# Optimization experiments

Hardware: AMD Instinct MI355X
Metric: run time of the kernel (lower is better)

Reference implementation:

```python
import jax, jax.numpy as jnp
import numpy as np

N = 50000
E = 800000
D_IN_X = 128
D_IN = 256   # concat(x, state)
D_OUT = 128
H_EDGE = 16
EW_MAX = 5.0
EPS = 1e-06


def setup_inputs() -> dict:
    key = jax.random.key(0)
    ks = jax.random.split(key, 10)
    x = jax.random.normal(ks[0], (N, D_IN_X), dtype=jnp.float32)
    state = jax.random.normal(ks[1], (N, D_IN_X), dtype=jnp.float32)
    edge_index = jax.random.randint(ks[2], (2, E), 0, N, dtype=jnp.int64)
    edge_weight = jax.random.uniform(ks[3], (E,), dtype=jnp.float32)
    s_in = 1.0 / np.sqrt(D_IN)
    s_h = 1.0 / np.sqrt(D_OUT)
    s_o = 1.0 / np.sqrt(H_EDGE)
    W_in = jax.random.uniform(ks[4], (D_IN, D_OUT), jnp.float32, -s_in, s_in)
    b_in = jax.random.uniform(ks[5], (D_OUT,), jnp.float32, -s_in, s_in)
    W1 = jax.random.uniform(ks[6], (D_OUT, H_EDGE), jnp.float32, -s_h, s_h)
    b1 = jax.random.uniform(ks[7], (H_EDGE,), jnp.float32, -s_h, s_h)
    W2 = jax.random.uniform(ks[8], (H_EDGE, 1), jnp.float32, -s_o, s_o)
    b2 = jax.random.uniform(ks[9], (1,), jnp.float32, -s_o, s_o)
    return {"x": x, "state": state, "edge_index": edge_index, "edge_weight": edge_weight,
            "W_in": W_in, "b_in": b_in, "W1": W1, "b1": b1, "W2": W2, "b2": b2}


def reference(x, state, edge_index, edge_weight, W_in, b_in, W1, b1, W2, b2):
    n = x.shape[0]
    # node projection on concat(x, state): [N, D_OUT]
    x_proj = jnp.concatenate([x, state], axis=-1) @ W_in + b_in
    src = edge_index[0]
    dst = edge_index[1]
    msg = x_proj[src]                                   # [E, D_OUT] gather
    # dynamic edge gating: small MLP -> sigmoid -> softplus window
    h = jax.nn.leaky_relu(msg @ W1 + b1, 0.1)           # [E, 16]
    w_dyn = jax.nn.sigmoid(h @ W2 + b2)                 # [E, 1]
    w = edge_weight[:, None] * jax.nn.softplus(4.0 * (w_dyn - 0.5))
    w = jnp.clip(w, 0.0, EW_MAX)                        # (second clamp is a no-op)
    msg = msg * w
    # scatter-add aggregation + degree normalization
    out = jax.ops.segment_sum(msg, dst, num_segments=n)
    deg = jax.ops.segment_sum(jnp.abs(w), dst, num_segments=n)
    out = out / (deg + EPS)
    out = out + x_proj                                  # residual (dims match)
    out = jax.nn.gelu(out, approximate=False)           # torch nn.GELU default = exact
    return out
```

## Files before the change

kernel.cpp:

```cpp
#include <hip/hip_runtime.h>
#include <hip/hip_fp16.h>
#include <math.h>

#define NN 50000
#define NE 800000
#define DD 128
#define KIN 256
#define SCAN_BLOCKS ((NN + 255) / 256)
#define GATE_BLOCKS ((NN + 63) / 64)
#define WCONV_BLOCKS 136
#define EDGE_BLOCKS (NE / 256)

typedef __attribute__((ext_vector_type(8))) short short8;
typedef __attribute__((ext_vector_type(4))) float f32x4;

__device__ __forceinline__ float gelu_exact(float v) {
    return 0.5f * v * (1.0f + erff(v * 0.7071067811865476f));
}
__device__ __forceinline__ unsigned short f2bf(float f) {
    unsigned int u = __float_as_uint(f);
    unsigned int r = (u + 0x7fffu + ((u >> 16) & 1u)) >> 16;
    return (unsigned short)r;
}
__device__ __forceinline__ float bfhi(unsigned int v) { return __uint_as_float(v & 0xffff0000u); }
__device__ __forceinline__ float bflo(unsigned int v) { return __uint_as_float(v << 16); }

__device__ __forceinline__ unsigned pack_sw(int src, float w) {
    unsigned short h = __half_as_ushort(__float2half_rn(w));
    return ((unsigned)src << 16) | (unsigned)h;
}
__device__ __forceinline__ float unpack_w(unsigned sw) {
    return __half2float(__ushort_as_half((unsigned short)(sw & 0xffffu)));
}

__global__ __launch_bounds__(256) void prep_kernel(
    const float* __restrict__ W, const float* __restrict__ W1,
    unsigned short* __restrict__ Wt, unsigned short* __restrict__ W1t,
    const int* __restrict__ ei, int* __restrict__ hist8)
{
    const int bid = blockIdx.x, t = threadIdx.x;
    if (bid < WCONV_BLOCKS) {
        int idx = bid * 256 + t;
        if (idx < 128 * 256) {
            int c = idx >> 8, k = idx & 255;
            Wt[idx] = f2bf(W[k * 128 + c]);
        } else if (idx < 128 * 256 + 16 * 128) {
            int i = idx - 128 * 256;
            int j = i >> 7, k = i & 127;
            W1t[i] = f2bf(W1[k * 16 + j]);
        }
    } else {
        int bid2 = bid - WCONV_BLOCKS;
        int e = bid2 * 256 + t;
        int part = bid2 & 7;
        atomicAdd(&hist8[part * NN + ei[NE + e]], 1);
    }
}

__global__ __launch_bounds__(256) void proj_mfma_kernel(
    const float* __restrict__ x, const float* __restrict__ st,
    const unsigned short* __restrict__ Wt, const float* __restrict__ b,
    unsigned short* __restrict__ xpb)
{
    __shared__ unsigned short Ald[64 * 256];
    __shared__ unsigned short Bld[128 * 128];
    const int t = threadIdx.x;
    const int lane = t & 63;
    const int w = t >> 6;
    const int row0 = blockIdx.x * 64;

    #pragma unroll
    for (int i = 0; i < 8; ++i) {
        int r = i * 8 + (t >> 5);
        int kf = (t & 31) * 8;
        int grow = row0 + r;
        float v[8];
        if (grow < NN) {
            const float* src = (kf < 128) ? &x[(size_t)grow * 128 + kf]
                                          : &st[(size_t)grow * 128 + (kf - 128)];
            float4 p0 = *(const float4*)src;
            float4 p1 = *(const float4*)(src + 4);
            v[0]=p0.x; v[1]=p0.y; v[2]=p0.z; v[3]=p0.w;
            v[4]=p1.x; v[5]=p1.y; v[6]=p1.z; v[7]=p1.w;
        } else {
            #pragma unroll
            for (int j = 0; j < 8; ++j) v[j] = 0.f;
        }
        short8 h;
        #pragma unroll
        for (int j = 0; j < 8; ++j) h[j] = (short)f2bf(v[j]);
        int byte = (r * 512 + kf * 2) ^ ((r & 7) << 4);
        *(short8*)((char*)Ald + byte) = h;
    }

    auto stageB = [&](int kh) {
        #pragma unroll
        for (int i = 0; i < 8; ++i) {
            int c  = i * 16 + (t >> 4);
            int kq = (t & 15) * 8;
            short8 vv = *(const short8*)&Wt[c * 256 + kh * 128 + kq];
            int byte = (c * 256 + kq * 2) ^ ((c & 7) << 4);
            *(short8*)((char*)Bld + byte) = vv;
        }
    };
    stageB(0);
    __syncthreads();

    f32x4 acc[8];
    #pragma unroll
    for (int ct = 0; ct < 8; ++ct) acc[ct] = (f32x4){0.f, 0.f, 0.f, 0.f};

    const int arow = w * 16 + (lane & 15);
    const int kgrp = (lane >> 4) * 8;
    const int cl   = lane & 15;

    #pragma unroll
    for (int kh = 0; kh < 2; ++kh) {
        if (kh == 1) {
            __syncthreads();
            stageB(1);
            __syncthreads();
        }
        #pragma unroll
        for (int k0 = 0; k0 < 128; k0 += 32) {
            int ka = kh * 128 + k0 + kgrp;
            int abyte = (arow * 512 + ka * 2) ^ ((arow & 7) << 4);
            short8 av = *(short8*)((char*)Ald + abyte);
            #pragma unroll
            for (int ct = 0; ct < 8; ++ct) {
                int c = ct * 16 + cl;
                int bbyte = (c * 256 + (k0 + kgrp) * 2) ^ ((c & 7) << 4);
                short8 bv = *(short8*)((char*)Bld + bbyte);
                acc[ct] = __builtin_amdgcn_mfma_f32_16x16x32_bf16(av, bv, acc[ct], 0, 0, 0);
            }
        }
    }

    const int rbase = row0 + w * 16 + ((lane >> 4) << 2);
    #pragma unroll
    for (int ct = 0; ct < 8; ++ct) {
        int col = ct * 16 + cl;
        float bias = b[col];
        #pragma unroll
        for (int r = 0; r < 4; ++r) {
            int row = rbase + r;
            if (row < NN)
                xpb[(size_t)row * 128 + col] = f2bf(acc[ct][r] + bias);
        }
    }
}

__global__ __launch_bounds__(256) void gate_scan_kernel(
    const unsigned short* __restrict__ xpb, const unsigned short* __restrict__ W1t,
    const float* __restrict__ b1, const float* __restrict__ W2,
    const float* __restrict__ b2, float* __restrict__ f,
    const int* __restrict__ hist8, int* __restrict__ row_start, int* __restrict__ bsum)
{
    __shared__ int lds[256];
    const int t = threadIdx.x;
    if (blockIdx.x < GATE_BLOCKS) {
        const int lane = t & 63, w = t >> 6;
        const int base = blockIdx.x * 64 + w * 16;
        if (base >= NN) return;
        const int m  = lane & 15;
        const int kg = (lane >> 4) * 8;

        int arow = base + m;
        if (arow >= NN) arow = NN - 1;
        const unsigned short* ap = &xpb[(size_t)arow * 128 + kg];
        const unsigned short* bp = &W1t[m * 128 + kg];

        f32x4 acc = (f32x4){0.f, 0.f, 0.f, 0.f};
        #pragma unroll
        for (int k0 = 0; k0 < 4; ++k0) {
            short8 av = *(const short8*)(ap + k0 * 32);
            short8 bv = *(const short8*)(bp + k0 * 32);
            acc = __builtin_amdgcn_mfma_f32_16x16x32_bf16(av, bv, acc, 0, 0, 0);
        }

        const float bias = b1[m];
        const float w2   = W2[m];
        float zp[4];
        #pragma unroll
        for (int r = 0; r < 4; ++r) {
            float h = acc[r] + bias;
            h = (h > 0.f) ? h : 0.1f * h;
            zp[r] = h * w2;
        }
        #pragma unroll
        for (int off = 1; off <= 8; off <<= 1) {
            #pragma unroll
            for (int r = 0; r < 4; ++r)
                zp[r] += __shfl_xor(zp[r], off);
        }
        if (m == 0) {
            const float bb2 = b2[0];
            #pragma unroll
            for (int r = 0; r < 4; ++r) {
                int node = base + ((lane >> 4) << 2) + r;
                if (node < NN) {
                    float z   = zp[r] + bb2;
                    float wd  = 1.f / (1.f + expf(-z));
                    float arg = 4.f * (wd - 0.5f);
                    f[node] = log1pf(expf(arg));
                }
            }
        }
    } else {
        const int sbid = blockIdx.x - GATE_BLOCKS;
        int i = sbid * 256 + t;
        int v = 0;
        if (i < NN) {
            #pragma unroll
            for (int k = 0; k < 8; ++k) v += hist8[k * NN + i];
        }
        lds[t] = v;
        __syncthreads();
        #pragma unroll
        for (int off = 1; off < 256; off <<= 1) {
            int u = (t >= off) ? lds[t - off] : 0;
            __syncthreads();
            lds[t] += u;
            __syncthreads();
        }
        if (i < NN) row_start[i] = lds[t] - v;
        if (t == 255) bsum[sbid] = lds[255];
    }
}

__global__ __launch_bounds__(256) void scan3_kernel(
    int* __restrict__ row_start, const int* __restrict__ bsum,
    int* __restrict__ hist8 , int* __restrict__ row_end)
{
    __shared__ int lds[256];
    const int t = threadIdx.x;
    int v = (t < SCAN_BLOCKS) ? bsum[t] : 0;
    lds[t] = v;
    __syncthreads();
    #pragma unroll
    for (int off = 1; off < 256; off <<= 1) {
        int u = (t >= off) ? lds[t - off] : 0;
        __syncthreads();
        lds[t] += u;
        __syncthreads();
    }
    int boff = (blockIdx.x == 0) ? 0 : lds[blockIdx.x - 1];
    int i = blockIdx.x * 256 + t;
    if (i < NN) {
        int run = row_start[i] + boff;
        row_start[i] = run;
        #pragma unroll
        for (int k = 0; k < 8; ++k) {
            int h = hist8[k * NN + i];
            hist8[k * NN + i] = run;
            run += h;
        }
        row_end[i] = run;
    }
}

__global__ __launch_bounds__(256) void scatter_kernel(
    const int* __restrict__ ei, const float* __restrict__ ew,
    const float* __restrict__ f, int* __restrict__ cursor8,
    unsigned* __restrict__ sw_s)
{
    int e = blockIdx.x * 256 + threadIdx.x;
    int part = blockIdx.x & 7;
    int src = ei[e];
    int dst = ei[NE + e];
    float w = fminf(ew[e] * f[src], 5.0f);
    int pos = atomicAdd(&cursor8[part * NN + dst], 1);
    sw_s[pos] = pack_sw(src, w);
}

__global__ __launch_bounds__(256) void aggregate_kernel(
    const int* __restrict__ row_start, const int* __restrict__ row_end,
    const unsigned* __restrict__ sw_s, const unsigned short* __restrict__ xpb,
    float* __restrict__ out)
{
    const int wid = threadIdx.x >> 6, lane = threadIdx.x & 63;
    const int g = lane >> 4;
    const int s16 = lane & 15;
    const int n = blockIdx.x * 4 + wid;
    if (n >= NN) return;
    const int beg = row_start[n], end = row_end[n];

    float a0=0.f,a1=0.f,a2=0.f,a3=0.f,a4=0.f,a5=0.f,a6=0.f,a7=0.f,deg=0.f;

    #pragma unroll 4
    for (int i = beg; i < end; i += 4) {
        int idx = i + g;
        int idc = (idx < NE) ? idx : (NE - 1);
        unsigned sw = sw_s[idc];
        float w = (idx < end) ? unpack_w(sw) : 0.f;
        uint4 v = *(const uint4*)&xpb[(size_t)(sw >> 16) * 128 + s16 * 8];
        a0 = fmaf(bflo(v.x), w, a0);
        a1 = fmaf(bfhi(v.x), w, a1);
        a2 = fmaf(bflo(v.y), w, a2);
        a3 = fmaf(bfhi(v.y), w, a3);
        a4 = fmaf(bflo(v.z), w, a4);
        a5 = fmaf(bfhi(v.z), w, a5);
        a6 = fmaf(bflo(v.w), w, a6);
        a7 = fmaf(bfhi(v.w), w, a7);
        deg += w;
    }
    #pragma unroll
    for (int off = 16; off <= 32; off <<= 1) {
        a0 += __shfl_xor(a0, off); a1 += __shfl_xor(a1, off);
        a2 += __shfl_xor(a2, off); a3 += __shfl_xor(a3, off);
        a4 += __shfl_xor(a4, off); a5 += __shfl_xor(a5, off);
        a6 += __shfl_xor(a6, off); a7 += __shfl_xor(a7, off);
        deg += __shfl_xor(deg, off);
    }

    float inv = 1.f / (deg + 1e-6f);
    float e0 = (g == 0) ? a0 : (g == 1) ? a2 : (g == 2) ? a4 : a6;
    float e1 = (g == 0) ? a1 : (g == 1) ? a3 : (g == 2) ? a5 : a7;
    unsigned int rv = *(const unsigned int*)&xpb[(size_t)n * 128 + s16 * 8 + g * 2];
    float2 o;
    o.x = gelu_exact(fmaf(e0, inv, bflo(rv)));
    o.y = gelu_exact(fmaf(e1, inv, bfhi(rv)));
    *(float2*)&out[(size_t)n * 128 + s16 * 8 + g * 2] = o;
}

extern "C" void kernel_launch(void* const* d_in, const int* in_sizes, int n_in,
                              void* d_out, int out_size, void* d_ws, size_t ws_size,
                              hipStream_t stream)
{
    const float* x    = (const float*)d_in[0];
    const float* st   = (const float*)d_in[1];
    const int*   ei   = (const int*)d_in[2];
    const float* ew   = (const float*)d_in[3];
    const float* W_in = (const float*)d_in[4];
    const float* b_in = (const float*)d_in[5];
    const float* W1   = (const float*)d_in[6];
    const float* b1   = (const float*)d_in[7];
    const float* W2   = (const float*)d_in[8];
    const float* b2   = (const float*)d_in[9];
    float* out = (float*)d_out;

    unsigned short* xpb = (unsigned short*)d_ws;
    float* f         = (float*)(xpb + (size_t)NN * 128);
    int*   row_end   = (int*)(f + NN);
    int*   row_start = row_end + NN;
    int*   bsum      = row_start + NN;
    int*   hist8     = bsum + 256;
    unsigned* sw_s   = (unsigned*)(hist8 + 8 * NN);
    unsigned short* Wt  = (unsigned short*)(sw_s + NE);
    unsigned short* W1t = Wt + 128 * 256;

    hipMemsetAsync(hist8, 0, 8 * NN * sizeof(int), stream);

    hipLaunchKernelGGL(prep_kernel, dim3(WCONV_BLOCKS + EDGE_BLOCKS), dim3(256), 0, stream,
                       W_in, W1, Wt, W1t, ei, hist8);
    hipLaunchKernelGGL(proj_mfma_kernel, dim3((NN + 63) / 64), dim3(256), 0, stream,
                       x, st, Wt, b_in, xpb);
    hipLaunchKernelGGL(gate_scan_kernel, dim3(GATE_BLOCKS + SCAN_BLOCKS), dim3(256), 0, stream,
                       xpb, W1t, b1, W2, b2, f, hist8, row_start, bsum);
    hipLaunchKernelGGL(scan3_kernel, dim3(SCAN_BLOCKS), dim3(256), 0, stream,
                       row_start, bsum, hist8, row_end);
    hipLaunchKernelGGL(scatter_kernel, dim3(EDGE_BLOCKS), dim3(256), 0, stream,
                       ei, ew, f, hist8, sw_s);
    hipLaunchKernelGGL(aggregate_kernel, dim3((NN + 3) / 4), dim3(256), 0, stream,
                       row_start, row_end, sw_s, xpb, out);
}
```

Baseline: 242.7 us.

## Replace global-atomic CSR build with two-pass bucketed LDS radix sort

Replaces the per-node global atomic histogram, multi-kernel scan and atomic scatter with a two-level bucket sort. Edges are first binned by dst>>8 into fixed-capacity staging buckets using LDS histograms. A second kernel then sorts each bucket locally in shared memory, emits row_start/row_end, and writes the packed src/weight records. This cuts global atomics, the memset of the 8xN histogram and two kernel launches. The cost is an extra 8-byte-per-edge staging pass, and a fixed CAP of 4608 per bucket that could overflow on skewed degree distributions.

Result: faster. 196.8 us (-18.9%).

```diff
diff --git a/kernel.cpp b/kernel.cpp
--- a/kernel.cpp
+++ b/kernel.cpp
@@ -6,10 +6,12 @@
 #define NE 800000
 #define DD 128
 #define KIN 256
-#define SCAN_BLOCKS ((NN + 255) / 256)
 #define GATE_BLOCKS ((NN + 63) / 64)
 #define WCONV_BLOCKS 136
-#define EDGE_BLOCKS (NE / 256)
+#define NB 196
+#define CAP 4608
+#define SA_BLOCKS 256
+#define EPB (NE / SA_BLOCKS)
 
 typedef __attribute__((ext_vector_type(8))) short short8;
 typedef __attribute__((ext_vector_type(4))) float f32x4;
@@ -36,7 +38,8 @@
 __global__ __launch_bounds__(256) void prep_kernel(
     const float* __restrict__ W, const float* __restrict__ W1,
     unsigned short* __restrict__ Wt, unsigned short* __restrict__ W1t,
-    const int* __restrict__ ei, int* __restrict__ hist8)
+    const int* __restrict__ ei, const float* __restrict__ ew,
+    int* __restrict__ bucket_cnt, uint2* __restrict__ stage)
 {
     const int bid = blockIdx.x, t = threadIdx.x;
     if (bid < WCONV_BLOCKS) {
@@ -49,11 +52,33 @@
             int j = i >> 7, k = i & 127;
             W1t[i] = f2bf(W1[k * 16 + j]);
         }
-    } else {
-        int bid2 = bid - WCONV_BLOCKS;
-        int e = bid2 * 256 + t;
-        int part = bid2 & 7;
-        atomicAdd(&hist8[part * NN + ei[NE + e]], 1);
+        return;
+    }
+    __shared__ int hist[NB];
+    __shared__ int basel[NB];
+    const int bid2 = bid - WCONV_BLOCKS;
+    const int e0 = bid2 * EPB, e1 = e0 + EPB;
+
+    for (int i = t; i < NB; i += 256) hist[i] = 0;
+    __syncthreads();
+    for (int e = e0 + t; e < e1; e += 256)
+        atomicAdd(&hist[ei[NE + e] >> 8], 1);
+    __syncthreads();
+    for (int i = t; i < NB; i += 256)
+        basel[i] = atomicAdd(&bucket_cnt[i], hist[i]);
+    __syncthreads();
+    for (int i = t; i < NB; i += 256) hist[i] = 0;
+    __syncthreads();
+    for (int e = e0 + t; e < e1; e += 256) {
+        int dst = ei[NE + e];
+        int src = ei[e];
+        float w = ew[e];
+        int b = dst >> 8;
+        int r = atomicAdd(&hist[b], 1);
+        uint2 rec;
+        rec.x = (unsigned)src | ((unsigned)(dst & 255) << 16);
+        rec.y = __float_as_uint(w);
+        stage[(size_t)b * CAP + basel[b] + r] = rec;
     }
 }
 
@@ -150,127 +175,122 @@
     }
 }
 
-__global__ __launch_bounds__(256) void gate_scan_kernel(
+__global__ __launch_bounds__(256) void gate_kernel(
     const unsigned short* __restrict__ xpb, const unsigned short* __restrict__ W1t,
     const float* __restrict__ b1, const float* __restrict__ W2,
-    const float* __restrict__ b2, float* __restrict__ f,
-    const int* __restrict__ hist8, int* __restrict__ row_start, int* __restrict__ bsum)
-{
-    __shared__ int lds[256];
-    const int t = threadIdx.x;
-    if (blockIdx.x < GATE_BLOCKS) {
-        const int lane = t & 63, w = t >> 6;
-        const int base = blockIdx.x * 64 + w * 16;
-        if (base >= NN) return;
-        const int m  = lane & 15;
-        const int kg = (lane >> 4) * 8;
-
-        int arow = base + m;
-        if (arow >= NN) arow = NN - 1;
-        const unsigned short* ap = &xpb[(size_t)arow * 128 + kg];
-        const unsigned short* bp = &W1t[m * 128 + kg];
-
-        f32x4 acc = (f32x4){0.f, 0.f, 0.f, 0.f};
-        #pragma unroll
-        for (int k0 = 0; k0 < 4; ++k0) {
-            short8 av = *(const short8*)(ap + k0 * 32);
-            short8 bv = *(const short8*)(bp + k0 * 32);
-            acc = __builtin_amdgcn_mfma_f32_16x16x32_bf16(av, bv, acc, 0, 0, 0);
-        }
-
-        const float bias = b1[m];
-        const float w2   = W2[m];
-        float zp[4];
+    const float* __restrict__ b2, float* __restrict__ f)
+{
+    const int t = threadIdx.x, lane = t & 63, w = t >> 6;
+    const int base = blockIdx.x * 64 + w * 16;
+    if (base >= NN) return;
+    const int m  = lane & 15;
+    const int kg = (lane >> 4) * 8;
+
+    int arow = base + m;
+    if (arow >= NN) arow = NN - 1;
+    const unsigned short* ap = &xpb[(size_t)arow * 128 + kg];
+    const unsigned short* bp = &W1t[m * 128 + kg];
+
+    f32x4 acc = (f32x4){0.f, 0.f, 0.f, 0.f};
+    #pragma unroll
+    for (int k0 = 0; k0 < 4; ++k0) {
+        short8 av = *(const short8*)(ap + k0 * 32);
+        short8 bv = *(const short8*)(bp + k0 * 32);
+        acc = __builtin_amdgcn_mfma_f32_16x16x32_bf16(av, bv, acc, 0, 0, 0);
+    }
+
+    const float bias = b1[m];
+    const float w2   = W2[m];
+    float zp[4];
+    #pragma unroll
+    for (int r = 0; r < 4; ++r) {
+        float h = acc[r] + bias;
+        h = (h > 0.f) ? h : 0.1f * h;
+        zp[r] = h * w2;
+    }
+    #pragma unroll
+    for (int off = 1; off <= 8; off <<= 1) {
+        #pragma unroll
+        for (int r = 0; r < 4; ++r)
+            zp[r] += __shfl_xor(zp[r], off);
+    }
+    if (m == 0) {
+        const float bb2 = b2[0];
         #pragma unroll
         for (int r = 0; r < 4; ++r) {
-            float h = acc[r] + bias;
-            h = (h > 0.f) ? h : 0.1f * h;
-            zp[r] = h * w2;
-        }
-        #pragma unroll
-        for (int off = 1; off <= 8; off <<= 1) {
-            #pragma unroll
-            for (int r = 0; r < 4; ++r)
-                zp[r] += __shfl_xor(zp[r], off);
-        }
-        if (m == 0) {
-            const float bb2 = b2[0];
-            #pragma unroll
-            for (int r = 0; r < 4; ++r) {
-                int node = base + ((lane >> 4) << 2) + r;
-                if (node < NN) {
-                    float z   = zp[r] + bb2;
-                    float wd  = 1.f / (1.f + expf(-z));
-                    float arg = 4.f * (wd - 0.5f);
-                    f[node] = log1pf(expf(arg));
-                }
+            int node = base + ((lane >> 4) << 2) + r;
+            if (node < NN) {
+                float z   = zp[r] + bb2;
+                float wd  = 1.f / (1.f + expf(-z));
+                float arg = 4.f * (wd - 0.5f);
+                f[node] = log1pf(expf(arg));
             }
         }
-    } else {
-        const int sbid = blockIdx.x - GATE_BLOCKS;
-        int i = sbid * 256 + t;
-        int v = 0;
-        if (i < NN) {
-            #pragma unroll
-            for (int k = 0; k < 8; ++k) v += hist8[k * NN + i];
-        }
-        lds[t] = v;
+    }
+}
+
+__global__ __launch_bounds__(256) void stageB_kernel(
+    const uint2* __restrict__ stage, const int* __restrict__ bucket_cnt,
+    const float* __restrict__ f, unsigned* __restrict__ sw_s,
+    int* __restrict__ row_start, int* __restrict__ row_end)
+{
+    __shared__ int pref[256];
+    __shared__ int hist[256];
+    __shared__ int off[256];
+    __shared__ int cur[256];
+    __shared__ unsigned sorted[CAP];
+    const int b = blockIdx.x, t = threadIdx.x;
+
+    int c = (t < NB) ? bucket_cnt[t] : 0;
+    pref[t] = c;
+    __syncthreads();
+    #pragma unroll
+    for (int o = 1; o < 256; o <<= 1) {
+        int u = (t >= o) ? pref[t - o] : 0;
         __syncthreads();
-        #pragma unroll
-        for (int off = 1; off < 256; off <<= 1) {
-            int u = (t >= off) ? lds[t - off] : 0;
-            __syncthreads();
-            lds[t] += u;
-            __syncthreads();
-        }
-        if (i < NN) row_start[i] = lds[t] - v;
-        if (t == 255) bsum[sbid] = lds[255];
-    }
-}
-
-__global__ __launch_bounds__(256) void scan3_kernel(
-    int* __restrict__ row_start, const int* __restrict__ bsum,
-    int* __restrict__ hist8 , int* __restrict__ row_end)
-{
-    __shared__ int lds[256];
-    const int t = threadIdx.x;
-    int v = (t < SCAN_BLOCKS) ? bsum[t] : 0;
-    lds[t] = v;
-    __syncthreads();
-    #pragma unroll
-    for (int off = 1; off < 256; off <<= 1) {
-        int u = (t >= off) ? lds[t - off] : 0;
+        pref[t] += u;
         __syncthreads();
-        lds[t] += u;
+    }
+    const int base_b = (b == 0) ? 0 : pref[b - 1];
+    const int cnt = bucket_cnt[b];
+
+    hist[t] = 0;
+    __syncthreads();
+    const uint2* sb = &stage[(size_t)b * CAP];
+    for (int i = t; i < cnt; i += 256)
+        atomicAdd(&hist[(sb[i].x >> 16) & 255], 1);
+    __syncthreads();
+    int h = hist[t];
+    pref[t] = h;
+    __syncthreads();
+    #pragma unroll
+    for (int o = 1; o < 256; o <<= 1) {
+        int u = (t >= o) ? pref[t - o] : 0;
         __syncthreads();
-    }
-    int boff = (blockIdx.x == 0) ? 0 : lds[blockIdx.x - 1];
-    int i = blockIdx.x * 256 + t;
-    if (i < NN) {
-        int run = row_start[i] + boff;
-        row_start[i] = run;
-        #pragma unroll
-        for (int k = 0; k < 8; ++k) {
-            int h = hist8[k * NN + i];
-            hist8[k * NN + i] = run;
-            run += h;
-        }
-        row_end[i] = run;
-    }
-}
-
-__global__ __launch_bounds__(256) void scatter_kernel(
-    const int* __restrict__ ei, const float* __restrict__ ew,
-    const float* __restrict__ f, int* __restrict__ cursor8,
-    unsigned* __restrict__ sw_s)
-{
-    int e = blockIdx.x * 256 + threadIdx.x;
-    int part = blockIdx.x & 7;
-    int src = ei[e];
-    int dst = ei[NE + e];
-    float w = fminf(ew[e] * f[src], 5.0f);
-    int pos = atomicAdd(&cursor8[part * NN + dst], 1);
-    sw_s[pos] = pack_sw(src, w);
+        pref[t] += u;
+        __syncthreads();
+    }
+    off[t] = pref[t] - h;
+    cur[t] = 0;
+    __syncthreads();
+
+    int node = b * 256 + t;
+    if (node < NN) {
+        row_start[node] = base_b + off[t];
+        row_end[node]   = base_b + off[t] + h;
+    }
+
+    for (int i = t; i < cnt; i += 256) {
+        uint2 rec = sb[i];
+        int src = rec.x & 0xffff;
+        int dl  = (rec.x >> 16) & 255;
+        float w = fminf(__uint_as_float(rec.y) * f[src], 5.0f);
+        int r = atomicAdd(&cur[dl], 1);
+        sorted[off[dl] + r] = pack_sw(src, w);
+    }
+    __syncthreads();
+    for (int i = t; i < cnt; i += 256)
+        sw_s[base_b + i] = sorted[i];
 }
 
 __global__ __launch_bounds__(256) void aggregate_kernel(
@@ -340,27 +360,25 @@
     float* out = (float*)d_out;
 
     unsigned short* xpb = (unsigned short*)d_ws;
-    float* f         = (float*)(xpb + (size_t)NN * 128);
-    int*   row_end   = (int*)(f + NN);
-    int*   row_start = row_end + NN;
-    int*   bsum      = row_start + NN;
-    int*   hist8     = bsum + 256;
-    unsigned* sw_s   = (unsigned*)(hist8 + 8 * NN);
+    float* f          = (float*)(xpb + (size_t)NN * 128);
+    int*   row_start  = (int*)(f + NN);
+    int*   row_end    = row_start + NN;
+    int*   bucket_cnt = row_end + NN;
+    uint2* stage      = (uint2*)(bucket_cnt + 256);
+    unsigned* sw_s    = (unsigned*)(stage + (size_t)NB * CAP);
     unsigned short* Wt  = (unsigned short*)(sw_s + NE);
     unsigned short* W1t = Wt + 128 * 256;
 
-    hipMemsetAsync(hist8, 0, 8 * NN * sizeof(int), stream);
-
-    hipLaunchKernelGGL(prep_kernel, dim3(WCONV_BLOCKS + EDGE_BLOCKS), dim3(256), 0, stream,
-                       W_in, W1, Wt, W1t, ei, hist8);
+    hipMemsetAsync(bucket_cnt, 0, 256 * sizeof(int), stream);
+
+    hipLaunchKernelGGL(prep_kernel, dim3(WCONV_BLOCKS + SA_BLOCKS), dim3(256), 0, stream,
+                       W_in, W1, Wt, W1t, ei, ew, bucket_cnt, stage);
     hipLaunchKernelGGL(proj_mfma_kernel, dim3((NN + 63) / 64), dim3(256), 0, stream,
                        x, st, Wt, b_in, xpb);
-    hipLaunchKernelGGL(gate_scan_kernel, dim3(GATE_BLOCKS + SCAN_BLOCKS), dim3(256), 0, stream,
-                       xpb, W1t, b1, W2, b2, f, hist8, row_start, bsum);
-    hipLaunchKernelGGL(scan3_kernel, dim3(SCAN_BLOCKS), dim3(256), 0, stream,
-                       row_start, bsum, hist8, row_end);
-    hipLaunchKernelGGL(scatter_kernel, dim3(EDGE_BLOCKS), dim3(256), 0, stream,
-                       ei, ew, f, hist8, sw_s);
+    hipLaunchKernelGGL(gate_kernel, dim3(GATE_BLOCKS), dim3(256), 0, stream,
+                       xpb, W1t, b1, W2, b2, f);
+    hipLaunchKernelGGL(stageB_kernel, dim3(NB), dim3(256), 0, stream,
+                       stage, bucket_cnt, f, sw_s, row_start, row_end);
     hipLaunchKernelGGL(aggregate_kernel, dim3((NN + 3) / 4), dim3(256), 0, stream,
                        row_start, row_end, sw_s, xpb, out);
 }
```
